# Performance work log

Hardware: AMD Instinct MI355X
Metric: run time of the kernel (lower is better)

The kernel has to match this reference:

```python
import jax, jax.numpy as jnp
import numpy as np

B, NPG, E, D, H = 64, 4096, 4194304, 384, 32
N = B * NPG

def setup_inputs() -> dict:
    key = jax.random.key(0)
    ks = jax.random.split(key, 10)
    x = jax.random.normal(ks[0], (N, D), jnp.float32)
    edge_index = jax.random.randint(ks[1], (2, E), 0, N, dtype=jnp.int32)
    batch = jnp.repeat(jnp.arange(B, dtype=jnp.int32), NPG)
    s = 0.05
    W1 = jax.random.normal(ks[2], (D, H), jnp.float32) * s
    b1 = jnp.zeros((H,), jnp.float32)
    W2 = jax.random.normal(ks[3], (H, 8), jnp.float32) * s
    b2 = jnp.zeros((8,), jnp.float32)
    W3 = jax.random.normal(ks[4], (8, 8), jnp.float32) * s
    b3 = jnp.zeros((8,), jnp.float32)
    W4 = jax.random.normal(ks[5], (8, 2), jnp.float32) * s
    b4 = jnp.zeros((2,), jnp.float32)
    return {"x": x, "edge_index": edge_index, "batch": batch,
            "W1": W1, "b1": b1, "W2": W2, "b2": b2,
            "W3": W3, "b3": b3, "W4": W4, "b4": b4}

def _leaky(v):
    return jnp.where(v > 0, v, 0.2 * v)

def reference(x, edge_index, batch, W1, b1, W2, b2, W3, b3, W4, b4):
    n = x.shape[0]
    loop = jnp.arange(n, dtype=edge_index.dtype)
    src = jnp.concatenate([edge_index[0], loop])  # [E+N]
    dst = jnp.concatenate([edge_index[1], loop])
    # GCN symmetric normalization with self-loops (edge_weight = 1)
    deg = jax.ops.segment_sum(jnp.ones(src.shape[0], jnp.float32), dst, num_segments=n)
    dis = jnp.where(deg > 0, jax.lax.rsqrt(jnp.maximum(deg, 1.0)), 0.0)
    norm = (dis[src] * dis[dst])[:, None]  # [E+N, 1]

    def gcn(h, W, b):
        h = h @ W                                   # project first (PyG order)
        agg = jax.ops.segment_sum(h[src] * norm, dst, num_segments=n)
        return agg + b

    h = _leaky(gcn(x, W1, b1))   # [N, 32]
    h = _leaky(gcn(h, W2, b2))   # [N, 8]
    bs = int(np.asarray(batch).max()) + 1
    g = jnp.mean(h.reshape(bs, -1, h.shape[-1]), axis=1)  # mean readout [B, 8]
    g = _leaky(g @ W3 + b3)      # lin1 + leaky_relu; dropout is identity (eval)
    return g @ W4 + b4           # [B, 2]
```

## Files before the change

### kernel.cpp

```cpp
#include <hip/hip_runtime.h>
#include <cstdint>

__device__ __forceinline__ float leaky(float v) { return v > 0.f ? v : 0.2f * v; }
__device__ __forceinline__ unsigned short f2bf(float f) {
  unsigned int u = __float_as_uint(f);
  unsigned int r = (u + 0x7FFFu + ((u >> 16) & 1u)) >> 16;
  return (unsigned short)r;
}
__device__ __forceinline__ float bf2f(unsigned short h) {
  return __uint_as_float(((unsigned int)h) << 16);
}

#define NPB 512

__global__ __launch_bounds__(256) void k_bin1(const int* __restrict__ dst,
                                              int* __restrict__ counts,
                                              int E, int CHUNK, int NBKT, int NBLK1) {
  __shared__ int hist[NPB];
  int t = threadIdx.x;
  int blk = blockIdx.x;
  for (int i = t; i < NBKT; i += 256) hist[i] = 0;
  __syncthreads();
  int e0 = blk * CHUNK;
  int e1 = min(e0 + CHUNK, E);
  for (int e = e0 + t; e < e1; e += 256) atomicAdd(&hist[dst[e] >> 9], 1);
  __syncthreads();
  for (int i = t; i < NBKT; i += 256) counts[i * NBLK1 + blk] = hist[i];
}

__global__ __launch_bounds__(256) void k_scan1(const int* __restrict__ cnt,
                                               int* __restrict__ bsums) {
  __shared__ int red[256];
  int t = threadIdx.x;
  int base = blockIdx.x * 1024;
  int s = cnt[base + t] + cnt[base + t + 256] + cnt[base + t + 512] + cnt[base + t + 768];
  red[t] = s;
  __syncthreads();
  for (int off = 128; off > 0; off >>= 1) {
    if (t < off) red[t] += red[t + off];
    __syncthreads();
  }
  if (t == 0) bsums[blockIdx.x] = red[0];
}

__global__ __launch_bounds__(256) void k_scan2(int* __restrict__ bsums, int* __restrict__ S,
                                               int total, int E, int nb) {
  __shared__ int sc[256];
  int t = threadIdx.x;
  int v = (t < nb) ? bsums[t] : 0;
  sc[t] = v;
  __syncthreads();
  for (int off = 1; off < 256; off <<= 1) {
    int u = (t >= off) ? sc[t - off] : 0;
    __syncthreads();
    sc[t] += u;
    __syncthreads();
  }
  if (t < nb) bsums[t] = (t == 0) ? 0 : sc[t - 1];
  if (t == 0) S[total] = E;
}

__global__ __launch_bounds__(256) void k_scan3(const int* __restrict__ cnt,
                                               const int* __restrict__ bsums,
                                               int* __restrict__ S) {
  __shared__ int sc[256];
  int t = threadIdx.x;
  int base = blockIdx.x * 1024;
  int4 d = *(const int4*)(cnt + base + 4 * t);
  int tot = d.x + d.y + d.z + d.w;
  sc[t] = tot;
  __syncthreads();
  for (int off = 1; off < 256; off <<= 1) {
    int u = (t >= off) ? sc[t - off] : 0;
    __syncthreads();
    sc[t] += u;
    __syncthreads();
  }
  int toff = bsums[blockIdx.x] + ((t == 0) ? 0 : sc[t - 1]);
  int4 ro;
  ro.x = toff;
  ro.y = toff + d.x;
  ro.z = toff + d.x + d.y;
  ro.w = toff + d.x + d.y + d.z;
  *(int4*)(S + base + 4 * t) = ro;
}

__global__ __launch_bounds__(256) void k_bin2(const int* __restrict__ ei,
                                              const int* __restrict__ S,
                                              int* __restrict__ binned,
                                              int E, int CHUNK, int NBKT, int NBLK1) {
  __shared__ int cur[NPB];
  int t = threadIdx.x;
  int blk = blockIdx.x;
  for (int i = t; i < NBKT; i += 256) cur[i] = S[i * NBLK1 + blk];
  __syncthreads();
  int e0 = blk * CHUNK;
  int e1 = min(e0 + CHUNK, E);
  for (int e = e0 + t; e < e1; e += 256) {
    int s = ei[e];
    int d = ei[E + e];
    int pos = atomicAdd(&cur[d >> 9], 1);
    binned[pos] = (s << 9) | (d & 511);
  }
}

__global__ __launch_bounds__(256) void k_build(const int* __restrict__ binned,
                                               const int* __restrict__ S,
                                               int* __restrict__ row_off,
                                               float* __restrict__ dis,
                                               int* __restrict__ csr,
                                               int E, int N, int NBKT, int NBLK1) {
  __shared__ int h[NPB];
  __shared__ int cur[NPB];
  int t = threadIdx.x;
  int b = blockIdx.x;
  int node0 = b * NPB;
  int begb = S[b * NBLK1];
  int endb = (b + 1 < NBKT) ? S[(b + 1) * NBLK1] : E;
  for (int i = t; i < NPB; i += 256) h[i] = 0;
  __syncthreads();
  for (int e = begb + t; e < endb; e += 256) atomicAdd(&h[binned[e] & 511], 1);
  __syncthreads();
  for (int off = 1; off < NPB; off <<= 1) {
    int i0 = t, i1 = t + 256;
    int a0 = (i0 >= off) ? h[i0 - off] : 0;
    int a1 = (i1 >= off) ? h[i1 - off] : 0;
    __syncthreads();
    h[i0] += a0;
    h[i1] += a1;
    __syncthreads();
  }
  for (int i = t; i < NPB; i += 256) {
    int incl = h[i];
    int excl = i ? h[i - 1] : 0;
    row_off[node0 + i] = begb + excl;
    cur[i] = excl;
    dis[node0 + i] = rsqrtf((float)(incl - excl + 1));
  }
  __syncthreads();
  for (int e = begb + t; e < endb; e += 256) {
    int ed = binned[e];
    int pos = atomicAdd(&cur[ed & 511], 1);
    csr[begb + pos] = ed >> 9;
  }
  if (b == NBKT - 1 && t == 0) row_off[N] = E;
}


__global__ __launch_bounds__(256) void k_gemm1(const float* __restrict__ x,
                                               const float* __restrict__ W1,
                                               unsigned short* __restrict__ h1b) {
  __shared__ float xl[32 * 256];
  __shared__ float wl[32 * 32];
  int t = threadIdx.x;
  size_t n0 = (size_t)blockIdx.x * 256;
  int fg8 = (t & 3) * 8;
  int ng4 = (t >> 2) * 4;
  float acc[4][8];
#pragma unroll
  for (int i = 0; i < 4; i++)
#pragma unroll
    for (int c = 0; c < 8; c++) acc[i][c] = 0.f;

  for (int kc = 0; kc < 384; kc += 32) {
    __syncthreads();
#pragma unroll
    for (int g = 0; g < 2; g++) {
      float4 v[4];
#pragma unroll
      for (int i = 0; i < 4; i++) {
        int idx = g * 1024 + i * 256 + t;
        int k4 = idx & 7;
        int n = idx >> 3;
        v[i] = *(const float4*)(x + (n0 + n) * 384 + kc + k4 * 4);
      }
#pragma unroll
      for (int i = 0; i < 4; i++) {
        int idx = g * 1024 + i * 256 + t;
        int k4 = idx & 7;
        int n = idx >> 3;
        xl[(k4 * 4 + 0) * 256 + n] = v[i].x;
        xl[(k4 * 4 + 1) * 256 + n] = v[i].y;
        xl[(k4 * 4 + 2) * 256 + n] = v[i].z;
        xl[(k4 * 4 + 3) * 256 + n] = v[i].w;
      }
    }
    ((float4*)wl)[t] = ((const float4*)(W1 + kc * 32))[t];
    __syncthreads();
#pragma unroll
    for (int k = 0; k < 32; k++) {
      float4 xv = *(const float4*)&xl[k * 256 + ng4];
      float4 wa = *(const float4*)&wl[k * 32 + fg8];
      float4 wb = *(const float4*)&wl[k * 32 + fg8 + 4];
      float xr[4] = {xv.x, xv.y, xv.z, xv.w};
      float wr[8] = {wa.x, wa.y, wa.z, wa.w, wb.x, wb.y, wb.z, wb.w};
#pragma unroll
      for (int i = 0; i < 4; i++)
#pragma unroll
        for (int c = 0; c < 8; c++) acc[i][c] = fmaf(xr[i], wr[c], acc[i][c]);
    }
  }
#pragma unroll
  for (int i = 0; i < 4; i++) {
    uint4 pk;
    pk.x = (unsigned)f2bf(acc[i][0]) | ((unsigned)f2bf(acc[i][1]) << 16);
    pk.y = (unsigned)f2bf(acc[i][2]) | ((unsigned)f2bf(acc[i][3]) << 16);
    pk.z = (unsigned)f2bf(acc[i][4]) | ((unsigned)f2bf(acc[i][5]) << 16);
    pk.w = (unsigned)f2bf(acc[i][6]) | ((unsigned)f2bf(acc[i][7]) << 16);
    *(uint4*)(h1b + (n0 + ng4 + i) * 32 + fg8) = pk;
  }
}


__global__ __launch_bounds__(256) void k_agg1_fused(const unsigned short* __restrict__ h1b,
                                                    const float* __restrict__ dis,
                                                    const int* __restrict__ row_off,
                                                    const int* __restrict__ csr,
                                                    const float* __restrict__ b1,
                                                    const float* __restrict__ W2,
                                                    unsigned short* __restrict__ h2b) {
  __shared__ float w2s[256];
  int t = threadIdx.x;
  w2s[t] = W2[t];
  __syncthreads();
  int lane = t & 63;
  int half = lane >> 5;
  int j = lane & 31;
  int n = blockIdx.x * 4 + (t >> 6);
  int beg = row_off[n], end = row_off[n + 1];
  float dn = dis[n];
  float acc = half ? 0.f : bf2f(h1b[(size_t)n * 32 + j]) * dn;
  int p = beg + half;
  for (; p + 6 < end; p += 8) {
    int s0 = csr[p], s1 = csr[p + 2], s2 = csr[p + 4], s3 = csr[p + 6];
    float d0 = dis[s0], d1 = dis[s1], d2 = dis[s2], d3 = dis[s3];
    float v0 = bf2f(h1b[(size_t)s0 * 32 + j]);
    float v1 = bf2f(h1b[(size_t)s1 * 32 + j]);
    float v2 = bf2f(h1b[(size_t)s2 * 32 + j]);
    float v3 = bf2f(h1b[(size_t)s3 * 32 + j]);
    acc += v0 * d0 + v1 * d1 + v2 * d2 + v3 * d3;
  }
  for (; p < end; p += 2) {
    int s = csr[p];
    acc += bf2f(h1b[(size_t)s * 32 + j]) * dis[s];
  }
  acc += __shfl_xor(acc, 32);
  float o = leaky(acc * dn + b1[j]);
  float pr[8];
#pragma unroll
  for (int c = 0; c < 8; c++) pr[c] = o * w2s[j * 8 + c];
#pragma unroll
  for (int off = 1; off < 32; off <<= 1) {
#pragma unroll
    for (int c = 0; c < 8; c++) pr[c] += __shfl_xor(pr[c], off);
  }
  if (lane == 0) {
    uint4 pk;
    pk.x = (unsigned)f2bf(pr[0]) | ((unsigned)f2bf(pr[1]) << 16);
    pk.y = (unsigned)f2bf(pr[2]) | ((unsigned)f2bf(pr[3]) << 16);
    pk.z = (unsigned)f2bf(pr[4]) | ((unsigned)f2bf(pr[5]) << 16);
    pk.w = (unsigned)f2bf(pr[6]) | ((unsigned)f2bf(pr[7]) << 16);
    *(uint4*)(h2b + (size_t)n * 8) = pk;
  }
}


__global__ __launch_bounds__(256) void k_agg2r(const unsigned short* __restrict__ h2b,
                                               const float* __restrict__ dis,
                                               const int* __restrict__ row_off,
                                               const int* __restrict__ csr,
                                               const float* __restrict__ b2,
                                               float* __restrict__ gbuf, int NPG) {
  __shared__ float red[128];
  int t = threadIdx.x;
  int j = t & 7;
  int sub = (t >> 3) & 1;
  int nl = t >> 4;
  int n = blockIdx.x * 16 + nl;
  int beg = row_off[n], end = row_off[n + 1];
  float dn = dis[n];
  float acc = sub ? 0.f : bf2f(h2b[(size_t)n * 8 + j]) * dn;
  int p = beg + sub;
  for (; p + 6 < end; p += 8) {
    int s0 = csr[p], s1 = csr[p + 2], s2 = csr[p + 4], s3 = csr[p + 6];
    float d0 = dis[s0], d1 = dis[s1], d2 = dis[s2], d3 = dis[s3];
    float v0 = bf2f(h2b[(size_t)s0 * 8 + j]);
    float v1 = bf2f(h2b[(size_t)s1 * 8 + j]);
    float v2 = bf2f(h2b[(size_t)s2 * 8 + j]);
    float v3 = bf2f(h2b[(size_t)s3 * 8 + j]);
    acc += v0 * d0 + v1 * d1 + v2 * d2 + v3 * d3;
  }
  for (; p < end; p += 2) {
    int s = csr[p];
    acc += bf2f(h2b[(size_t)s * 8 + j]) * dis[s];
  }
  acc += __shfl_xor(acc, 8);
  if (sub == 0) red[nl * 8 + j] = leaky(acc * dn + b2[j]);
  __syncthreads();
  if (t < 8) {
    float s = 0.f;
#pragma unroll
    for (int i = 0; i < 16; i++) s += red[i * 8 + t];
    int graph = (blockIdx.x * 16) / NPG;
    atomicAdd(&gbuf[graph * 8 + t], s);
  }
}


__global__ __launch_bounds__(64) void k_mlp(const float* __restrict__ g,
                                            const float* __restrict__ W3,
                                            const float* __restrict__ b3,
                                            const float* __restrict__ W4,
                                            const float* __restrict__ b4,
                                            float* __restrict__ out, int B, int NPG) {
  int b = threadIdx.x;
  if (b >= B) return;
  float inv = 1.0f / (float)NPG;
  float gi[8], t1[8];
#pragma unroll
  for (int k = 0; k < 8; k++) gi[k] = g[b * 8 + k] * inv;
#pragma unroll
  for (int jj = 0; jj < 8; jj++) {
    float s = b3[jj];
#pragma unroll
    for (int k = 0; k < 8; k++) s = fmaf(gi[k], W3[k * 8 + jj], s);
    t1[jj] = leaky(s);
  }
#pragma unroll
  for (int jj = 0; jj < 2; jj++) {
    float s = b4[jj];
#pragma unroll
    for (int k = 0; k < 8; k++) s = fmaf(t1[k], W4[k * 2 + jj], s);
    out[b * 2 + jj] = s;
  }
}

extern "C" void kernel_launch(void* const* d_in, const int* in_sizes, int n_in,
                              void* d_out, int out_size, void* d_ws, size_t ws_size,
                              hipStream_t stream) {
  const float* x  = (const float*)d_in[0];
  const int*   ei = (const int*)d_in[1];
  const float* W1 = (const float*)d_in[3];
  const float* b1 = (const float*)d_in[4];
  const float* W2 = (const float*)d_in[5];
  const float* b2 = (const float*)d_in[6];
  const float* W3 = (const float*)d_in[7];
  const float* b3 = (const float*)d_in[8];
  const float* W4 = (const float*)d_in[9];
  const float* b4 = (const float*)d_in[10];

  const int E = in_sizes[1] / 2;
  const int N = in_sizes[2];
  const int B = out_size / 2;
  const int NPG = N / B;

  const int NBKT  = N / NPB;
  const int NBLK1 = 512;
  const int CHUNK = (E + NBLK1 - 1) / NBLK1;
  const int SCN   = NBKT * NBLK1;
  const int NBS   = SCN / 1024;

  size_t off = 0;
  auto place = [&](size_t bytes) {
    size_t p = off;
    off = (off + bytes + 255) & ~(size_t)255;
    return p;
  };
  size_t o_counts  = place((size_t)SCN * 4);
  size_t o_S       = place(((size_t)SCN + 1) * 4);
  size_t o_bsums   = place(1024 * 4);
  size_t o_dis     = place((size_t)N * 4);
  size_t o_row_off = place(((size_t)N + 1) * 4);
  size_t o_csr     = place((size_t)E * 4);
  size_t o_binned  = place((size_t)E * 4 > (size_t)N * 64 ? (size_t)E * 4 : (size_t)N * 64);
  size_t o_h2      = place((size_t)N * 8 * 2);
  size_t o_gbuf    = place((size_t)B * 8 * 4);
  if (off > ws_size || N % NPB != 0) {
    hipMemsetAsync(d_out, 0, (size_t)out_size * 4, stream);
    return;
  }
  char* ws = (char*)d_ws;
  int*   counts  = (int*)(ws + o_counts);
  int*   S       = (int*)(ws + o_S);
  int*   bsums   = (int*)(ws + o_bsums);
  float* dis     = (float*)(ws + o_dis);
  int*   row_off = (int*)(ws + o_row_off);
  int*   csr     = (int*)(ws + o_csr);
  int*   binned  = (int*)(ws + o_binned);
  unsigned short* h1b = (unsigned short*)(ws + o_binned);
  unsigned short* h2b = (unsigned short*)(ws + o_h2);
  float* gbuf    = (float*)(ws + o_gbuf);

  hipMemsetAsync(gbuf, 0, (size_t)B * 8 * 4, stream);
  k_bin1<<<NBLK1, 256, 0, stream>>>(ei + E, counts, E, CHUNK, NBKT, NBLK1);
  k_scan1<<<NBS, 256, 0, stream>>>(counts, bsums);
  k_scan2<<<1, 256, 0, stream>>>(bsums, S, SCN, E, NBS);
  k_scan3<<<NBS, 256, 0, stream>>>(counts, bsums, S);
  k_bin2<<<NBLK1, 256, 0, stream>>>(ei, S, binned, E, CHUNK, NBKT, NBLK1);
  k_build<<<NBKT, 256, 0, stream>>>(binned, S, row_off, dis, csr, E, N, NBKT, NBLK1);
  k_gemm1<<<N / 256, 256, 0, stream>>>(x, W1, h1b);
  k_agg1_fused<<<N / 4, 256, 0, stream>>>(h1b, dis, row_off, csr, b1, W2, h2b);
  k_agg2r<<<N / 16, 256, 0, stream>>>(h2b, dis, row_off, csr, b2, gbuf, NPG);
  k_mlp<<<1, 64, 0, stream>>>(gbuf, W3, b3, W4, b4, (float*)d_out, B, NPG);
}
```

Measured before the change: 966.9 us.

## Pack source degree scale into CSR entries and unroll aggregation loops deeper

The CSR build is split into two kernels so that dis is complete before edges are written. Each CSR entry then stores (src, dis[src]) as an int2. This removes the dependent random gather of dis[src] from both aggregation kernels, at the cost of doubling CSR storage and traffic plus one extra kernel launch that re-reads the binned edges. The aggregation loops are also unrolled to 8 edges per iteration, and 64-bit index math is dropped in favour of 32-bit, to expose more memory-level parallelism.

```diff
diff --git a/kernel.cpp b/kernel.cpp
--- a/kernel.cpp
+++ b/kernel.cpp
@@ -104,14 +104,12 @@
   }
 }
 
-__global__ __launch_bounds__(256) void k_build(const int* __restrict__ binned,
-                                               const int* __restrict__ S,
-                                               int* __restrict__ row_off,
-                                               float* __restrict__ dis,
-                                               int* __restrict__ csr,
-                                               int E, int N, int NBKT, int NBLK1) {
+__global__ __launch_bounds__(256) void k_build1(const int* __restrict__ binned,
+                                                const int* __restrict__ S,
+                                                int* __restrict__ row_off,
+                                                float* __restrict__ dis,
+                                                int E, int N, int NBKT, int NBLK1) {
   __shared__ int h[NPB];
-  __shared__ int cur[NPB];
   int t = threadIdx.x;
   int b = blockIdx.x;
   int node0 = b * NPB;
@@ -134,16 +132,31 @@
     int incl = h[i];
     int excl = i ? h[i - 1] : 0;
     row_off[node0 + i] = begb + excl;
-    cur[i] = excl;
     dis[node0 + i] = rsqrtf((float)(incl - excl + 1));
   }
+  if (b == NBKT - 1 && t == 0) row_off[N] = E;
+}
+
+__global__ __launch_bounds__(256) void k_build2(const int* __restrict__ binned,
+                                                const int* __restrict__ S,
+                                                const int* __restrict__ row_off,
+                                                const float* __restrict__ dis,
+                                                int2* __restrict__ csr2,
+                                                int E, int NBKT, int NBLK1) {
+  __shared__ int cur[NPB];
+  int t = threadIdx.x;
+  int b = blockIdx.x;
+  int node0 = b * NPB;
+  int begb = S[b * NBLK1];
+  int endb = (b + 1 < NBKT) ? S[(b + 1) * NBLK1] : E;
+  for (int i = t; i < NPB; i += 256) cur[i] = row_off[node0 + i] - begb;
   __syncthreads();
   for (int e = begb + t; e < endb; e += 256) {
     int ed = binned[e];
+    int s = ed >> 9;
     int pos = atomicAdd(&cur[ed & 511], 1);
-    csr[begb + pos] = ed >> 9;
-  }
-  if (b == NBKT - 1 && t == 0) row_off[N] = E;
+    csr2[begb + pos] = make_int2(s, __float_as_int(dis[s]));
+  }
 }
 
 
@@ -215,7 +228,7 @@
 __global__ __launch_bounds__(256) void k_agg1_fused(const unsigned short* __restrict__ h1b,
                                                     const float* __restrict__ dis,
                                                     const int* __restrict__ row_off,
-                                                    const int* __restrict__ csr,
+                                                    const int2* __restrict__ csr2,
                                                     const float* __restrict__ b1,
                                                     const float* __restrict__ W2,
                                                     unsigned short* __restrict__ h2b) {
@@ -229,20 +242,37 @@
   int n = blockIdx.x * 4 + (t >> 6);
   int beg = row_off[n], end = row_off[n + 1];
   float dn = dis[n];
-  float acc = half ? 0.f : bf2f(h1b[(size_t)n * 32 + j]) * dn;
+  float acc = half ? 0.f : bf2f(h1b[n * 32 + j]) * dn;
   int p = beg + half;
-  for (; p + 6 < end; p += 8) {
-    int s0 = csr[p], s1 = csr[p + 2], s2 = csr[p + 4], s3 = csr[p + 6];
-    float d0 = dis[s0], d1 = dis[s1], d2 = dis[s2], d3 = dis[s3];
-    float v0 = bf2f(h1b[(size_t)s0 * 32 + j]);
-    float v1 = bf2f(h1b[(size_t)s1 * 32 + j]);
-    float v2 = bf2f(h1b[(size_t)s2 * 32 + j]);
-    float v3 = bf2f(h1b[(size_t)s3 * 32 + j]);
-    acc += v0 * d0 + v1 * d1 + v2 * d2 + v3 * d3;
+  for (; p + 14 < end; p += 16) {
+    int2 e0 = csr2[p], e1 = csr2[p + 2], e2 = csr2[p + 4], e3 = csr2[p + 6];
+    int2 e4 = csr2[p + 8], e5 = csr2[p + 10], e6 = csr2[p + 12], e7 = csr2[p + 14];
+    float v0 = bf2f(h1b[e0.x * 32 + j]);
+    float v1 = bf2f(h1b[e1.x * 32 + j]);
+    float v2 = bf2f(h1b[e2.x * 32 + j]);
+    float v3 = bf2f(h1b[e3.x * 32 + j]);
+    float v4 = bf2f(h1b[e4.x * 32 + j]);
+    float v5 = bf2f(h1b[e5.x * 32 + j]);
+    float v6 = bf2f(h1b[e6.x * 32 + j]);
+    float v7 = bf2f(h1b[e7.x * 32 + j]);
+    acc += v0 * __int_as_float(e0.y) + v1 * __int_as_float(e1.y) +
+           v2 * __int_as_float(e2.y) + v3 * __int_as_float(e3.y) +
+           v4 * __int_as_float(e4.y) + v5 * __int_as_float(e5.y) +
+           v6 * __int_as_float(e6.y) + v7 * __int_as_float(e7.y);
+  }
+  if (p + 6 < end) {
+    int2 e0 = csr2[p], e1 = csr2[p + 2], e2 = csr2[p + 4], e3 = csr2[p + 6];
+    float v0 = bf2f(h1b[e0.x * 32 + j]);
+    float v1 = bf2f(h1b[e1.x * 32 + j]);
+    float v2 = bf2f(h1b[e2.x * 32 + j]);
+    float v3 = bf2f(h1b[e3.x * 32 + j]);
+    acc += v0 * __int_as_float(e0.y) + v1 * __int_as_float(e1.y) +
+           v2 * __int_as_float(e2.y) + v3 * __int_as_float(e3.y);
+    p += 8;
   }
   for (; p < end; p += 2) {
-    int s = csr[p];
-    acc += bf2f(h1b[(size_t)s * 32 + j]) * dis[s];
+    int2 ee = csr2[p];
+    acc += bf2f(h1b[ee.x * 32 + j]) * __int_as_float(ee.y);
   }
   acc += __shfl_xor(acc, 32);
   float o = leaky(acc * dn + b1[j]);
@@ -260,7 +290,7 @@
     pk.y = (unsigned)f2bf(pr[2]) | ((unsigned)f2bf(pr[3]) << 16);
     pk.z = (unsigned)f2bf(pr[4]) | ((unsigned)f2bf(pr[5]) << 16);
     pk.w = (unsigned)f2bf(pr[6]) | ((unsigned)f2bf(pr[7]) << 16);
-    *(uint4*)(h2b + (size_t)n * 8) = pk;
+    *(uint4*)(h2b + n * 8) = pk;
   }
 }
 
@@ -268,7 +298,7 @@
 __global__ __launch_bounds__(256) void k_agg2r(const unsigned short* __restrict__ h2b,
                                                const float* __restrict__ dis,
                                                const int* __restrict__ row_off,
-                                               const int* __restrict__ csr,
+                                               const int2* __restrict__ csr2,
                                                const float* __restrict__ b2,
                                                float* __restrict__ gbuf, int NPG) {
   __shared__ float red[128];
@@ -279,20 +309,37 @@
   int n = blockIdx.x * 16 + nl;
   int beg = row_off[n], end = row_off[n + 1];
   float dn = dis[n];
-  float acc = sub ? 0.f : bf2f(h2b[(size_t)n * 8 + j]) * dn;
+  float acc = sub ? 0.f : bf2f(h2b[n * 8 + j]) * dn;
   int p = beg + sub;
-  for (; p + 6 < end; p += 8) {
-    int s0 = csr[p], s1 = csr[p + 2], s2 = csr[p + 4], s3 = csr[p + 6];
-    float d0 = dis[s0], d1 = dis[s1], d2 = dis[s2], d3 = dis[s3];
-    float v0 = bf2f(h2b[(size_t)s0 * 8 + j]);
-    float v1 = bf2f(h2b[(size_t)s1 * 8 + j]);
-    float v2 = bf2f(h2b[(size_t)s2 * 8 + j]);
-    float v3 = bf2f(h2b[(size_t)s3 * 8 + j]);
-    acc += v0 * d0 + v1 * d1 + v2 * d2 + v3 * d3;
+  for (; p + 14 < end; p += 16) {
+    int2 e0 = csr2[p], e1 = csr2[p + 2], e2 = csr2[p + 4], e3 = csr2[p + 6];
+    int2 e4 = csr2[p + 8], e5 = csr2[p + 10], e6 = csr2[p + 12], e7 = csr2[p + 14];
+    float v0 = bf2f(h2b[e0.x * 8 + j]);
+    float v1 = bf2f(h2b[e1.x * 8 + j]);
+    float v2 = bf2f(h2b[e2.x * 8 + j]);
+    float v3 = bf2f(h2b[e3.x * 8 + j]);
+    float v4 = bf2f(h2b[e4.x * 8 + j]);
+    float v5 = bf2f(h2b[e5.x * 8 + j]);
+    float v6 = bf2f(h2b[e6.x * 8 + j]);
+    float v7 = bf2f(h2b[e7.x * 8 + j]);
+    acc += v0 * __int_as_float(e0.y) + v1 * __int_as_float(e1.y) +
+           v2 * __int_as_float(e2.y) + v3 * __int_as_float(e3.y) +
+           v4 * __int_as_float(e4.y) + v5 * __int_as_float(e5.y) +
+           v6 * __int_as_float(e6.y) + v7 * __int_as_float(e7.y);
+  }
+  if (p + 6 < end) {
+    int2 e0 = csr2[p], e1 = csr2[p + 2], e2 = csr2[p + 4], e3 = csr2[p + 6];
+    float v0 = bf2f(h2b[e0.x * 8 + j]);
+    float v1 = bf2f(h2b[e1.x * 8 + j]);
+    float v2 = bf2f(h2b[e2.x * 8 + j]);
+    float v3 = bf2f(h2b[e3.x * 8 + j]);
+    acc += v0 * __int_as_float(e0.y) + v1 * __int_as_float(e1.y) +
+           v2 * __int_as_float(e2.y) + v3 * __int_as_float(e3.y);
+    p += 8;
   }
   for (; p < end; p += 2) {
-    int s = csr[p];
-    acc += bf2f(h2b[(size_t)s * 8 + j]) * dis[s];
+    int2 ee = csr2[p];
+    acc += bf2f(h2b[ee.x * 8 + j]) * __int_as_float(ee.y);
   }
   acc += __shfl_xor(acc, 8);
   if (sub == 0) red[nl * 8 + j] = leaky(acc * dn + b2[j]);
@@ -371,7 +418,7 @@
   size_t o_bsums   = place(1024 * 4);
   size_t o_dis     = place((size_t)N * 4);
   size_t o_row_off = place(((size_t)N + 1) * 4);
-  size_t o_csr     = place((size_t)E * 4);
+  size_t o_csr2    = place((size_t)E * 8);
   size_t o_binned  = place((size_t)E * 4 > (size_t)N * 64 ? (size_t)E * 4 : (size_t)N * 64);
   size_t o_h2      = place((size_t)N * 8 * 2);
   size_t o_gbuf    = place((size_t)B * 8 * 4);
@@ -385,7 +432,7 @@
   int*   bsums   = (int*)(ws + o_bsums);
   float* dis     = (float*)(ws + o_dis);
   int*   row_off = (int*)(ws + o_row_off);
-  int*   csr     = (int*)(ws + o_csr);
+  int2*  csr2    = (int2*)(ws + o_csr2);
   int*   binned  = (int*)(ws + o_binned);
   unsigned short* h1b = (unsigned short*)(ws + o_binned);
   unsigned short* h2b = (unsigned short*)(ws + o_h2);
@@ -397,9 +444,10 @@
   k_scan2<<<1, 256, 0, stream>>>(bsums, S, SCN, E, NBS);
   k_scan3<<<NBS, 256, 0, stream>>>(counts, bsums, S);
   k_bin2<<<NBLK1, 256, 0, stream>>>(ei, S, binned, E, CHUNK, NBKT, NBLK1);
-  k_build<<<NBKT, 256, 0, stream>>>(binned, S, row_off, dis, csr, E, N, NBKT, NBLK1);
+  k_build1<<<NBKT, 256, 0, stream>>>(binned, S, row_off, dis, E, N, NBKT, NBLK1);
+  k_build2<<<NBKT, 256, 0, stream>>>(binned, S, row_off, dis, csr2, E, NBKT, NBLK1);
   k_gemm1<<<N / 256, 256, 0, stream>>>(x, W1, h1b);
-  k_agg1_fused<<<N / 4, 256, 0, stream>>>(h1b, dis, row_off, csr, b1, W2, h2b);
-  k_agg2r<<<N / 16, 256, 0, stream>>>(h2b, dis, row_off, csr, b2, gbuf, NPG);
+  k_agg1_fused<<<N / 4, 256, 0, stream>>>(h1b, dis, row_off, csr2, b1, W2, h2b);
+  k_agg2r<<<N / 16, 256, 0, stream>>>(h2b, dis, row_off, csr2, b2, gbuf, NPG);
   k_mlp<<<1, 64, 0, stream>>>(gbuf, W3, b3, W4, b4, (float*)d_out, B, NPG);
 }
```

After: 994.3 us. 2.8% more time.
